# Kernel optimization log

Measured on AMD Instinct MI355X. Metric: run time of the kernel, lower is better.

Reference implementation:

```python
import jax, jax.numpy as jnp
import numpy as np

N_NODES = 50000
N_EDGES = 800000
IN_DIM = 64
H_DIM = 64


def setup_inputs() -> dict:
    key = jax.random.key(0)
    ks = jax.random.split(key, 6)
    feat = jax.random.normal(ks[0], (N_NODES, IN_DIM), dtype=jnp.float32)
    W1 = jax.random.normal(ks[1], (IN_DIM, H_DIM), dtype=jnp.float32) * (1.0 / np.sqrt(IN_DIM))
    b1 = jnp.zeros((H_DIM,), dtype=jnp.float32)
    W2 = jax.random.normal(ks[2], (H_DIM, 1), dtype=jnp.float32) * (1.0 / np.sqrt(H_DIM))
    b2 = jnp.zeros((1,), dtype=jnp.float32)
    src = jax.random.randint(ks[3], (N_EDGES,), 0, N_NODES, dtype=jnp.int32)
    dst = jax.random.randint(ks[4], (N_EDGES,), 0, N_NODES, dtype=jnp.int32)
    return {"feat": feat, "W1": W1, "b1": b1, "W2": W2, "b2": b2, "src": src, "dst": dst}


def _norms(src, dst, n_nodes):
    # DGL GraphConv norm='both': symmetric D^{-1/2} A D^{-1/2}, degrees clamped to >=1
    ones = jnp.ones(src.shape[0], dtype=jnp.float32)
    out_deg = jax.ops.segment_sum(ones, src, num_segments=n_nodes)
    in_deg = jax.ops.segment_sum(ones, dst, num_segments=n_nodes)
    out_norm = jax.lax.rsqrt(jnp.clip(out_deg, 1.0))
    in_norm = jax.lax.rsqrt(jnp.clip(in_deg, 1.0))
    return out_norm, in_norm


def _graph_conv(feat, W, b, src, dst, out_norm, in_norm, act):
    h = feat * out_norm[:, None]          # scale source features by D_out^{-1/2}
    msg = h[src]                          # gather along edges [E, d]
    agg = jax.ops.segment_sum(msg, dst, num_segments=feat.shape[0])  # scatter-sum to dst
    agg = agg * in_norm[:, None]          # scale by D_in^{-1/2}
    return act(agg @ W + b)


def reference(feat, W1, b1, W2, b2, src, dst):
    out_norm, in_norm = _norms(src, dst, feat.shape[0])
    h = _graph_conv(feat, W1, b1, src, dst, out_norm, in_norm, jax.nn.relu)
    return _graph_conv(h, W2, b2, src, dst, out_norm, in_norm, jax.nn.sigmoid)
```

## Files before the change

### kernel.cpp

```cpp
#include <hip/hip_runtime.h>
#include <hip/hip_fp16.h>
#include <math.h>


#define BS 256
#define EPB 4096

__global__ void histA_featw1_kernel(const int* __restrict__ src, const int* __restrict__ dst,
                                    const float* __restrict__ feat, const float* __restrict__ W1,
                                    int* __restrict__ dstBinCount, int* __restrict__ srcBinCount,
                                    __half* __restrict__ featp,
                                    int E, int N, int NB, int T) {
    __shared__ float w[64 * 64];
    __shared__ int histD[256];
    __shared__ int histS[256];
    int tid = threadIdx.x;
    if ((int)blockIdx.x < T) {
        histD[tid] = 0; histS[tid] = 0;
        __syncthreads();
        int base = blockIdx.x * EPB;
        #pragma unroll
        for (int it = 0; it < EPB / BS; it++) {
            int e = base + it * BS + tid;
            if (e < E) {
                atomicAdd(&histD[dst[e] >> 8], 1);
                atomicAdd(&histS[src[e] >> 8], 1);
            }
        }
        __syncthreads();
        if (tid < NB) {
            if (histD[tid]) atomicAdd(&dstBinCount[tid], histD[tid]);
            if (histS[tid]) atomicAdd(&srcBinCount[tid], histS[tid]);
        }
    } else {
        for (int i = tid; i < 64 * 16; i += BS)
            ((float4*)w)[i] = ((const float4*)W1)[i];
        __syncthreads();
        int wave = tid >> 6, lane = tid & 63;
        int row = ((int)blockIdx.x - T) * 4 + wave;
        if (row >= N) return;
        const float4* fr = (const float4*)(feat + (size_t)row * 64);
        float acc = 0.0f;
        #pragma unroll
        for (int k4 = 0; k4 < 16; k4++) {
            float4 a = fr[k4];
            acc += a.x * w[(4 * k4 + 0) * 64 + lane];
            acc += a.y * w[(4 * k4 + 1) * 64 + lane];
            acc += a.z * w[(4 * k4 + 2) * 64 + lane];
            acc += a.w * w[(4 * k4 + 3) * 64 + lane];
        }
        featp[(size_t)row * 64 + lane] = __float2half(acc);
    }
}

__global__ void scan_bins_kernel(const int* __restrict__ dstBinCount, const int* __restrict__ srcBinCount,
                                 int* __restrict__ dstBinBase, int* __restrict__ srcBinBase,
                                 int* __restrict__ dstCursor, int* __restrict__ srcCursor, int NB) {
    __shared__ int s[256];
    int t = threadIdx.x;
    int v = (t < NB) ? dstBinCount[t] : 0;
    s[t] = v; __syncthreads();
    for (int off = 1; off < 256; off <<= 1) {
        int u = (t >= off) ? s[t - off] : 0; __syncthreads();
        s[t] += u; __syncthreads();
    }
    if (t < NB) {
        int ex = s[t] - v;
        dstBinBase[t] = ex; dstCursor[t] = ex;
        if (t == NB - 1) dstBinBase[NB] = s[t];
    }
    __syncthreads();
    v = (t < NB) ? srcBinCount[t] : 0;
    s[t] = v; __syncthreads();
    for (int off = 1; off < 256; off <<= 1) {
        int u = (t >= off) ? s[t - off] : 0; __syncthreads();
        s[t] += u; __syncthreads();
    }
    if (t < NB) {
        int ex = s[t] - v;
        srcBinBase[t] = ex; srcCursor[t] = ex;
        if (t == NB - 1) srcBinBase[NB] = s[t];
    }
}

__global__ void partition_kernel(const int* __restrict__ src, const int* __restrict__ dst,
                                 int* __restrict__ dstCursor, int* __restrict__ srcCursor,
                                 int* __restrict__ packed, int* __restrict__ srcPart,
                                 int E, int NB) {
    __shared__ int arr[256];
    int tid = threadIdx.x;
    int base = blockIdx.x * EPB;
    arr[tid] = 0; __syncthreads();
    #pragma unroll
    for (int it = 0; it < EPB / BS; it++) {
        int e = base + it * BS + tid;
        if (e < E) atomicAdd(&arr[dst[e] >> 8], 1);
    }
    __syncthreads();
    int h = arr[tid];
    int rb = (tid < NB && h) ? atomicAdd(&dstCursor[tid], h) : 0;
    __syncthreads();
    arr[tid] = rb;
    __syncthreads();
    #pragma unroll
    for (int it = 0; it < EPB / BS; it++) {
        int e = base + it * BS + tid;
        if (e < E) {
            int d = dst[e], s2 = src[e];
            int pos = atomicAdd(&arr[d >> 8], 1);
            packed[pos] = s2 | ((d & 255) << 17);
        }
    }
    __syncthreads();
    arr[tid] = 0; __syncthreads();
    #pragma unroll
    for (int it = 0; it < EPB / BS; it++) {
        int e = base + it * BS + tid;
        if (e < E) atomicAdd(&arr[src[e] >> 8], 1);
    }
    __syncthreads();
    h = arr[tid];
    rb = (tid < NB && h) ? atomicAdd(&srcCursor[tid], h) : 0;
    __syncthreads();
    arr[tid] = rb;
    __syncthreads();
    #pragma unroll
    for (int it = 0; it < EPB / BS; it++) {
        int e = base + it * BS + tid;
        if (e < E) {
            int s2 = src[e];
            int pos = atomicAdd(&arr[s2 >> 8], 1);
            srcPart[pos] = s2 & 255;
        }
    }
}

__global__ void finalize_kernel(const int* __restrict__ dstBinBase, const int* __restrict__ srcBinBase,
                                const int* __restrict__ packed, const int* __restrict__ srcPart,
                                int* __restrict__ csr_src, int* __restrict__ in_deg,
                                int* __restrict__ row_start, int* __restrict__ out_deg,
                                int N, int NB) {
    __shared__ int hist[256];
    __shared__ int sc[256];
    int tid = threadIdx.x;
    int b = blockIdx.x;
    if (b < NB) {
        int lo = dstBinBase[b], hi = dstBinBase[b + 1];
        hist[tid] = 0; __syncthreads();
        for (int i = lo + tid; i < hi; i += BS)
            atomicAdd(&hist[(packed[i] >> 17) & 255], 1);
        __syncthreads();
        int v = hist[tid];
        sc[tid] = v; __syncthreads();
        for (int off = 1; off < 256; off <<= 1) {
            int u = (tid >= off) ? sc[tid - off] : 0; __syncthreads();
            sc[tid] += u; __syncthreads();
        }
        int ex = sc[tid] - v;
        int n = b * 256 + tid;
        if (n < N) { in_deg[n] = v; row_start[n] = lo + ex; }
        sc[tid] = lo + ex;
        __syncthreads();
        for (int i = lo + tid; i < hi; i += BS) {
            int pv = packed[i];
            int pos = atomicAdd(&sc[(pv >> 17) & 255], 1);
            csr_src[pos] = pv & 0x1FFFF;
        }
    } else {
        int sb = b - NB;
        int lo = srcBinBase[sb], hi = srcBinBase[sb + 1];
        hist[tid] = 0; __syncthreads();
        for (int i = lo + tid; i < hi; i += BS)
            atomicAdd(&hist[srcPart[i]], 1);
        __syncthreads();
        int n = sb * 256 + tid;
        if (n < N) out_deg[n] = hist[tid];
    }
}

__global__ void csr_agg1_kernel(const int* __restrict__ row_start, const int* __restrict__ in_deg,
                                const int* __restrict__ csr_src, const int* __restrict__ out_deg,
                                const __half* __restrict__ featp,
                                const float* __restrict__ b1, const float* __restrict__ W2,
                                float* __restrict__ s_buf, int N) {
    int gid = blockIdx.x * blockDim.x + threadIdx.x;
    int n = gid >> 6;
    if (n >= N) return;
    int lane = threadIdx.x & 63;
    int g = lane >> 3;
    int l = lane & 7;
    int start = row_start[n];
    int deg = in_deg[n];
    float acc[8] = {0, 0, 0, 0, 0, 0, 0, 0};
    const uint4* fp4 = (const uint4*)featp;
    for (int j = 0; j < deg; j += 16) {
        int e0 = j + g;
        int e1 = j + 8 + g;
        bool p0 = e0 < deg;
        bool p1 = e1 < deg;
        int sn0 = p0 ? csr_src[start + e0] : 0;
        int sn1 = p1 ? csr_src[start + e1] : 0;
        uint4 q0 = {0, 0, 0, 0}, q1 = {0, 0, 0, 0};
        float on0 = 0.0f, on1 = 0.0f;
        if (p0) { q0 = fp4[(size_t)sn0 * 8 + l]; on0 = rsqrtf(fmaxf((float)out_deg[sn0], 1.0f)); }
        if (p1) { q1 = fp4[(size_t)sn1 * 8 + l]; on1 = rsqrtf(fmaxf((float)out_deg[sn1], 1.0f)); }
        const __half2* h0 = (const __half2*)&q0;
        const __half2* h1 = (const __half2*)&q1;
        #pragma unroll
        for (int c = 0; c < 4; c++) {
            float2 f0 = __half22float2(h0[c]);
            float2 f1 = __half22float2(h1[c]);
            acc[2 * c]     += on0 * f0.x + on1 * f1.x;
            acc[2 * c + 1] += on0 * f0.y + on1 * f1.y;
        }
    }
    #pragma unroll
    for (int off = 8; off < 64; off <<= 1) {
        #pragma unroll
        for (int c = 0; c < 8; c++)
            acc[c] += __shfl_xor(acc[c], off, 64);
    }
    float inn = rsqrtf(fmaxf((float)deg, 1.0f));
    float v = 0.0f;
    #pragma unroll
    for (int c = 0; c < 8; c++) {
        float h = fmaxf(inn * acc[c] + b1[l * 8 + c], 0.0f);
        v += h * W2[l * 8 + c];
    }
    #pragma unroll
    for (int off = 1; off < 8; off <<= 1)
        v += __shfl_xor(v, off, 64);
    if (lane == 0)
        s_buf[n] = rsqrtf(fmaxf((float)out_deg[n], 1.0f)) * v;
}

__global__ void csr_agg2_kernel(const int* __restrict__ row_start, const int* __restrict__ in_deg,
                                const int* __restrict__ csr_src,
                                const float* __restrict__ s_buf, const float* __restrict__ b2,
                                float* __restrict__ out, int N) {
    int gid = blockIdx.x * blockDim.x + threadIdx.x;
    int n = gid >> 4;
    if (n >= N) return;
    int sub = gid & 15;
    int start = row_start[n];
    int deg = in_deg[n];
    float a = 0.0f;
    for (int j = sub; j < deg; j += 32) {
        int j1 = j + 16;
        int i0 = csr_src[start + j];
        int i1 = (j1 < deg) ? csr_src[start + j1] : 0;
        float v0 = s_buf[i0];
        float v1 = (j1 < deg) ? s_buf[i1] : 0.0f;
        a += v0 + v1;
    }
    #pragma unroll
    for (int off = 1; off < 16; off <<= 1)
        a += __shfl_xor(a, off, 64);
    if (sub == 0) {
        float x = rsqrtf(fmaxf((float)deg, 1.0f)) * a + b2[0];
        out[n] = 1.0f / (1.0f + expf(-x));
    }
}

extern "C" void kernel_launch(void* const* d_in, const int* in_sizes, int n_in,
                              void* d_out, int out_size, void* d_ws, size_t ws_size,
                              hipStream_t stream) {
    const float* feat = (const float*)d_in[0];
    const float* W1   = (const float*)d_in[1];
    const float* b1   = (const float*)d_in[2];
    const float* W2   = (const float*)d_in[3];
    const float* b2   = (const float*)d_in[4];
    const int* src = (const int*)d_in[5];
    const int* dst = (const int*)d_in[6];
    float* out = (float*)d_out;

    const int N  = in_sizes[0] / 64;
    const int E  = in_sizes[5];
    const int NB = (N + 255) >> 8;
    const int T  = (E + EPB - 1) / EPB;

    int* wsi = (int*)d_ws;
    int* dstBinCount = wsi;
    int* srcBinCount = dstBinCount + NB;
    int* dstBinBase  = srcBinCount + NB;
    int* srcBinBase  = dstBinBase + NB + 1;
    int* dstCursor   = srcBinBase + NB + 1;
    int* srcCursor   = dstCursor + NB;
    int* in_deg      = srcCursor + NB;
    int* row_start   = in_deg + N;
    int* out_deg     = row_start + N;
    int* packed      = out_deg + N;
    int* srcPart     = packed + E;
    int* csr_src     = srcPart + E;
    size_t int_bytes = ((size_t)(6 * NB + 2) + 3 * (size_t)N + 3 * (size_t)E) * sizeof(int);
    size_t half_off  = (int_bytes + 15) & ~(size_t)15;
    __half* featp = (__half*)((char*)d_ws + half_off);
    float* s_buf  = (float*)((char*)d_ws + half_off + (size_t)64 * N * sizeof(__half));

    hipMemsetAsync(dstBinCount, 0, (size_t)2 * NB * sizeof(int), stream);

    histA_featw1_kernel<<<T + (N + 3) / 4, BS, 0, stream>>>(
        src, dst, feat, W1, dstBinCount, srcBinCount, featp, E, N, NB, T);
    scan_bins_kernel<<<1, 256, 0, stream>>>(
        dstBinCount, srcBinCount, dstBinBase, srcBinBase, dstCursor, srcCursor, NB);
    partition_kernel<<<T, BS, 0, stream>>>(
        src, dst, dstCursor, srcCursor, packed, srcPart, E, NB);
    finalize_kernel<<<2 * NB, BS, 0, stream>>>(
        dstBinBase, srcBinBase, packed, srcPart, csr_src, in_deg, row_start, out_deg, N, NB);
    csr_agg1_kernel<<<(int)(((size_t)N * 64 + BS - 1) / BS), BS, 0, stream>>>(
        row_start, in_deg, csr_src, out_deg, featp, b1, W2, s_buf, N);
    csr_agg2_kernel<<<(int)(((size_t)N * 16 + BS - 1) / BS), BS, 0, stream>>>(
        row_start, in_deg, csr_src, s_buf, b2, out, N);
}
```

Measured before the change: 185.4 us.

## Prescale fp16 features by out-degree norm and register-tile the W1 projection

The feat·W1 projection now keeps each lane's W1 column in registers and has every wave compute 16 rows, two at a time with split accumulators, so blocks no longer stage W1 through shared memory. The out-degree normalization is folded into the fp16 projected features inside the finalize kernel's source-degree blocks. This removes the per-edge out_deg gather and rsqrt from the first aggregation. In exchange it adds a read-modify-write pass over featp and a second fp16 rounding, and needs 64 weight registers per thread, which may reduce occupancy.

```diff
diff --git a/kernel.cpp b/kernel.cpp
--- a/kernel.cpp
+++ b/kernel.cpp
@@ -11,7 +11,6 @@
                                     int* __restrict__ dstBinCount, int* __restrict__ srcBinCount,
                                     __half* __restrict__ featp,
                                     int E, int N, int NB, int T) {
-    __shared__ float w[64 * 64];
     __shared__ int histD[256];
     __shared__ int histS[256];
     int tid = threadIdx.x;
@@ -33,23 +32,31 @@
             if (histS[tid]) atomicAdd(&srcBinCount[tid], histS[tid]);
         }
     } else {
-        for (int i = tid; i < 64 * 16; i += BS)
-            ((float4*)w)[i] = ((const float4*)W1)[i];
-        __syncthreads();
         int wave = tid >> 6, lane = tid & 63;
-        int row = ((int)blockIdx.x - T) * 4 + wave;
-        if (row >= N) return;
-        const float4* fr = (const float4*)(feat + (size_t)row * 64);
-        float acc = 0.0f;
-        #pragma unroll
-        for (int k4 = 0; k4 < 16; k4++) {
-            float4 a = fr[k4];
-            acc += a.x * w[(4 * k4 + 0) * 64 + lane];
-            acc += a.y * w[(4 * k4 + 1) * 64 + lane];
-            acc += a.z * w[(4 * k4 + 2) * 64 + lane];
-            acc += a.w * w[(4 * k4 + 3) * 64 + lane];
-        }
-        featp[(size_t)row * 64 + lane] = __float2half(acc);
+        float w[64];
+        #pragma unroll
+        for (int k = 0; k < 64; k++) w[k] = W1[k * 64 + lane];
+        int rowBase = ((int)blockIdx.x - T) * 64 + wave * 16;
+        #pragma unroll
+        for (int rr = 0; rr < 16; rr += 2) {
+            int row0 = rowBase + rr;
+            int row1 = row0 + 1;
+            const float4* f0 = (const float4*)(feat + (size_t)min(row0, N - 1) * 64);
+            const float4* f1 = (const float4*)(feat + (size_t)min(row1, N - 1) * 64);
+            float a0 = 0, a1 = 0, a2 = 0, a3 = 0;
+            float c0 = 0, c1 = 0, c2 = 0, c3 = 0;
+            #pragma unroll
+            for (int k4 = 0; k4 < 16; k4++) {
+                float4 x = f0[k4];
+                float4 y = f1[k4];
+                a0 += x.x * w[4 * k4 + 0]; a1 += x.y * w[4 * k4 + 1];
+                a2 += x.z * w[4 * k4 + 2]; a3 += x.w * w[4 * k4 + 3];
+                c0 += y.x * w[4 * k4 + 0]; c1 += y.y * w[4 * k4 + 1];
+                c2 += y.z * w[4 * k4 + 2]; c3 += y.w * w[4 * k4 + 3];
+            }
+            if (row0 < N) featp[(size_t)row0 * 64 + lane] = __float2half((a0 + a1) + (a2 + a3));
+            if (row1 < N) featp[(size_t)row1 * 64 + lane] = __float2half((c0 + c1) + (c2 + c3));
+        }
     }
 }
 
@@ -139,6 +146,7 @@
                                 const int* __restrict__ packed, const int* __restrict__ srcPart,
                                 int* __restrict__ csr_src, int* __restrict__ in_deg,
                                 int* __restrict__ row_start, int* __restrict__ out_deg,
+                                __half* __restrict__ featp,
                                 int N, int NB) {
     __shared__ int hist[256];
     __shared__ int sc[256];
@@ -174,7 +182,26 @@
             atomicAdd(&hist[srcPart[i]], 1);
         __syncthreads();
         int n = sb * 256 + tid;
-        if (n < N) out_deg[n] = hist[tid];
+        int od = hist[tid];
+        if (n < N) out_deg[n] = od;
+        float* snorm = (float*)sc;
+        snorm[tid] = rsqrtf(fmaxf((float)od, 1.0f));
+        __syncthreads();
+        int nodes = min(256, N - sb * 256);
+        uint4* fp = (uint4*)(featp + (size_t)sb * 256 * 64);
+        int total = nodes * 8;
+        for (int i = tid; i < total; i += BS) {
+            float s = snorm[i >> 3];
+            uint4 u = fp[i];
+            __half2* hh = (__half2*)&u;
+            #pragma unroll
+            for (int c = 0; c < 4; c++) {
+                float2 p = __half22float2(hh[c]);
+                p.x *= s; p.y *= s;
+                hh[c] = __float22half2_rn(p);
+            }
+            fp[i] = u;
+        }
     }
 }
 
@@ -201,17 +228,16 @@
         int sn0 = p0 ? csr_src[start + e0] : 0;
         int sn1 = p1 ? csr_src[start + e1] : 0;
         uint4 q0 = {0, 0, 0, 0}, q1 = {0, 0, 0, 0};
-        float on0 = 0.0f, on1 = 0.0f;
-        if (p0) { q0 = fp4[(size_t)sn0 * 8 + l]; on0 = rsqrtf(fmaxf((float)out_deg[sn0], 1.0f)); }
-        if (p1) { q1 = fp4[(size_t)sn1 * 8 + l]; on1 = rsqrtf(fmaxf((float)out_deg[sn1], 1.0f)); }
+        if (p0) q0 = fp4[(size_t)sn0 * 8 + l];
+        if (p1) q1 = fp4[(size_t)sn1 * 8 + l];
         const __half2* h0 = (const __half2*)&q0;
         const __half2* h1 = (const __half2*)&q1;
         #pragma unroll
         for (int c = 0; c < 4; c++) {
             float2 f0 = __half22float2(h0[c]);
             float2 f1 = __half22float2(h1[c]);
-            acc[2 * c]     += on0 * f0.x + on1 * f1.x;
-            acc[2 * c + 1] += on0 * f0.y + on1 * f1.y;
+            acc[2 * c]     += f0.x + f1.x;
+            acc[2 * c + 1] += f0.y + f1.y;
         }
     }
     #pragma unroll
@@ -299,14 +325,14 @@
 
     hipMemsetAsync(dstBinCount, 0, (size_t)2 * NB * sizeof(int), stream);
 
-    histA_featw1_kernel<<<T + (N + 3) / 4, BS, 0, stream>>>(
+    histA_featw1_kernel<<<T + (N + 63) / 64, BS, 0, stream>>>(
         src, dst, feat, W1, dstBinCount, srcBinCount, featp, E, N, NB, T);
     scan_bins_kernel<<<1, 256, 0, stream>>>(
         dstBinCount, srcBinCount, dstBinBase, srcBinBase, dstCursor, srcCursor, NB);
     partition_kernel<<<T, BS, 0, stream>>>(
         src, dst, dstCursor, srcCursor, packed, srcPart, E, NB);
     finalize_kernel<<<2 * NB, BS, 0, stream>>>(
-        dstBinBase, srcBinBase, packed, srcPart, csr_src, in_deg, row_start, out_deg, N, NB);
+        dstBinBase, srcBinBase, packed, srcPart, csr_src, in_deg, row_start, out_deg, featp, N, NB);
     csr_agg1_kernel<<<(int)(((size_t)N * 64 + BS - 1) / BS), BS, 0, stream>>>(
         row_start, in_deg, csr_src, out_deg, featp, b1, W2, s_buf, N);
     csr_agg2_kernel<<<(int)(((size_t)N * 16 + BS - 1) / BS), BS, 0, stream>>>(
```

Result: slower. 382.8 us (+106.5%).
